# Kernel tuning notes

Hardware: AMD Instinct MI355X
Metric: run time of the kernel (lower is better)

## Reference

```python
import jax, jax.numpy as jnp
import numpy as np

D, DC, DR, NH = 2048, 512, 64, 16
HD = D // NH
B, T = 2, 2048


def _rope_tables(sl, off, dr):
    inv = 1.0 / (10000.0 ** (jnp.arange(0, dr, 2, dtype=jnp.float32) / dr))
    t = jnp.arange(off, off + sl, dtype=jnp.float32)
    f = jnp.outer(t, inv)                      # [sl, dr/2]
    e = jnp.concatenate([f, f], -1)            # [sl, dr]
    return jnp.cos(e), jnp.sin(e)


def _rap(x, c, s):
    d = x.shape[-1]
    x1, x2 = x[..., : d // 2], x[..., d // 2:]
    ch, sh = c[..., : d // 2], s[..., : d // 2]
    return jnp.concatenate([x1 * ch - x2 * sh, x2 * ch + x1 * sh], -1)


def setup_inputs() -> dict:
    key = jax.random.key(0)
    ks = jax.random.split(key, 8)
    def w(k, i, o):
        return jax.random.normal(k, (i, o), jnp.float32) * (1.0 / np.sqrt(i))
    return {
        "x": jax.random.normal(ks[0], (B, T, D), jnp.float32),
        "Wkv": w(ks[1], D, DC),    # kv_down
        "Wkup": w(ks[2], DC, D),   # k_up
        "Wvup": w(ks[3], DC, D),   # v_up
        "Wq": w(ks[4], D, D),      # q_proj
        "Wqr": w(ks[5], D, DR),    # q_rope
        "Wkr": w(ks[6], DC, DR),   # k_rope
        "Wo": w(ks[7], D, D),      # o_proj
    }


def reference(x, Wkv, Wkup, Wvup, Wq, Wqr, Wkr, Wo):
    Bx, Tx, d = x.shape
    offset = 0
    ckv = x @ Wkv                                   # [B,T,dc]
    kr = ckv @ Wkr                                  # [B,T,dr]
    cos, sin = _rope_tables(Tx, offset, DR)         # [T,dr]
    kr = _rap(kr, cos[None], sin[None])
    entry = jnp.concatenate([ckv, kr], -1)          # [B,T,dc+dr] (kv cache entry)
    tl = entry.shape[1]

    k = (ckv @ Wkup).reshape(Bx, tl, NH, HD).transpose(0, 2, 1, 3)   # [B,H,tl,hd]
    v = (ckv @ Wvup).reshape(Bx, tl, NH, HD).transpose(0, 2, 1, 3)
    q = (x @ Wq).reshape(Bx, Tx, NH, HD).transpose(0, 2, 1, 3)        # [B,H,T,hd]

    qr = _rap(x @ Wqr, cos[None], sin[None])        # [B,T,dr]

    ac = jnp.einsum("bhtd,bhsd->bhts", q, k)        # content scores
    ar = jnp.einsum("btd,bsd->bts", qr, kr)         # shared RoPE scores (same per head)
    scale = np.sqrt(HD + DR).astype(np.float32)
    scores = (ac + ar[:, None]) / scale             # [B,H,T,tl]

    # causal mask: triu(-inf, diagonal=tl-T+1)
    i = jnp.arange(Tx)[:, None]
    j = jnp.arange(tl)[None, :]
    mask = j > i + (tl - Tx)
    scores = jnp.where(mask[None, None], -jnp.inf, scores)

    attn = jax.nn.softmax(scores, -1)
    out = jnp.einsum("bhts,bhsd->bhtd", attn, v).transpose(0, 2, 1, 3).reshape(Bx, Tx, -1)
    return out @ Wo, entry
```

## Files before the change

### kernel.cpp

```cpp
#include <hip/hip_runtime.h>
#include <math.h>
#include <type_traits>

#define D    2048
#define DC   512
#define DR   64
#define NH   16
#define HD   128
#define Bb   2
#define Tt   2048
#define ROWS (Bb*Tt)
#define LDX  2176

typedef __bf16 bf16x8 __attribute__((ext_vector_type(8)));
typedef __bf16 bf16x4 __attribute__((ext_vector_type(4)));
typedef float  f32x4  __attribute__((ext_vector_type(4)));

typedef const void __attribute__((address_space(1))) gvoid;
typedef void       __attribute__((address_space(3))) lvoid;

__device__ __forceinline__ void load_lds16(const void* g, void* l) {
    __builtin_amdgcn_global_load_lds((gvoid*)g, (lvoid*)l, 16, 0, 0);
}

template <bool WF32, bool WBF16>
__global__ __launch_bounds__(256)
void gemm_bt(const __bf16* __restrict__ A, const __bf16* __restrict__ BT,
             float* __restrict__ Cf, __bf16* __restrict__ Cb,
             int M, int K, int ldcf, int ldcb) {
    __shared__ __bf16 As[128 * 32];
    __shared__ __bf16 Bs[128 * 32];

    const int tid  = threadIdx.x;
    const int w    = tid >> 6;
    const int lane = tid & 63;
    const int quad = lane >> 4;
    const int lc   = lane & 15;
    const int bm   = blockIdx.y * 128;
    const int bn   = blockIdx.x * 128;
    const int wm   = (w & 1) * 64;
    const int wn   = (w >> 1) * 64;

    const int sr = w * 32 + (lane >> 2);
    const int sc = (lane & 3) * 8;

    f32x4 acc[4][4] = {};

    for (int k0 = 0; k0 < K; k0 += 32) {
        const __bf16* ga = A  + (size_t)(bm + sr) * K + k0 + sc;
        const __bf16* gb = BT + (size_t)(bn + sr) * K + k0 + sc;
        load_lds16(ga,                  &As[(w * 32) * 32]);
        load_lds16(ga + (size_t)16 * K, &As[(w * 32 + 16) * 32]);
        load_lds16(gb,                  &Bs[(w * 32) * 32]);
        load_lds16(gb + (size_t)16 * K, &Bs[(w * 32 + 16) * 32]);
        __syncthreads();

        bf16x8 af[4], bfr[4];
        #pragma unroll
        for (int mi = 0; mi < 4; ++mi)
            af[mi] = *(bf16x8*)&As[(wm + mi * 16 + lc) * 32 + quad * 8];
        #pragma unroll
        for (int ni = 0; ni < 4; ++ni)
            bfr[ni] = *(bf16x8*)&Bs[(wn + ni * 16 + lc) * 32 + quad * 8];
        #pragma unroll
        for (int mi = 0; mi < 4; ++mi)
            #pragma unroll
            for (int ni = 0; ni < 4; ++ni)
                acc[mi][ni] = __builtin_amdgcn_mfma_f32_16x16x32_bf16(
                    af[mi], bfr[ni], acc[mi][ni], 0, 0, 0);
        __syncthreads();
    }

    #pragma unroll
    for (int mi = 0; mi < 4; ++mi)
        #pragma unroll
        for (int r = 0; r < 4; ++r) {
            const int row = bm + wm + mi * 16 + quad * 4 + r;
            const int col = bn + wn + lc;
            #pragma unroll
            for (int ni = 0; ni < 4; ++ni) {
                float v = acc[mi][ni][r];
                if constexpr (WF32)  Cf[(size_t)row * ldcf + col + ni * 16] = v;
                if constexpr (WBF16) Cb[(size_t)row * ldcb + col + ni * 16] = (__bf16)v;
            }
        }
}

__global__ void f32_to_bf16(const float* __restrict__ in,
                            __bf16* __restrict__ out, int n) {
    int i = blockIdx.x * blockDim.x + threadIdx.x;
    if (i < n) out[i] = (__bf16)in[i];
}

__global__ __launch_bounds__(256)
void transpose_conv(const float* __restrict__ W, __bf16* __restrict__ WT,
                    int R, int C) {
    __shared__ float tile[64][65];
    const int r0 = blockIdx.x * 64;
    const int c0 = blockIdx.y * 64;
    const int tid = threadIdx.x;
    for (int e = tid; e < 64 * 64; e += 256) {
        int i = e >> 6, j = e & 63;
        tile[i][j] = W[(size_t)(r0 + i) * C + c0 + j];
    }
    __syncthreads();
    for (int e = tid; e < 64 * 64; e += 256) {
        int i = e >> 6, j = e & 63;
        WT[(size_t)(c0 + i) * R + r0 + j] = (__bf16)tile[j][i];
    }
}

__global__ void rope_ext(__bf16* __restrict__ p, float* __restrict__ ent) {
    int idx = blockIdx.x * blockDim.x + threadIdx.x;
    if (idx >= ROWS * 32) return;
    int row = idx >> 5;
    int i   = idx & 31;
    int t   = row & (Tt - 1);
    float inv  = powf(10000.0f, -(float)(2 * i) / 64.0f);
    float fr   = (float)t * inv;
    float c = cosf(fr), s = sinf(fr);
    __bf16* v = p + (size_t)row * LDX + 2048;
    float x1 = (float)v[i], x2 = (float)v[i + 32];
    float o1 = x1 * c - x2 * s;
    float o2 = x2 * c + x1 * s;
    v[i]      = (__bf16)o1;
    v[i + 32] = (__bf16)o2;
    if (ent) {
        ent[(size_t)row * 576 + 512 + i] = o1;
        ent[(size_t)row * 576 + 544 + i] = o2;
    }
}

__global__ __launch_bounds__(256)
void transpose_v(const __bf16* __restrict__ vb, __bf16* __restrict__ vtb) {
    __shared__ __bf16 tile[64][65];
    const int t0 = blockIdx.x * 64;
    const int c0 = blockIdx.y * 64;
    const int b  = blockIdx.z;
    const int tid = threadIdx.x;
    for (int e = tid; e < 64 * 64; e += 256) {
        int i = e >> 6, j = e & 63;
        tile[i][j] = vb[((size_t)(b * Tt + t0 + i)) * D + c0 + j];
    }
    __syncthreads();
    for (int e = tid; e < 64 * 64; e += 256) {
        int i = e >> 6, j = e & 63;
        vtb[((size_t)(b * D + c0 + i)) * Tt + t0 + j] = tile[j][i];
    }
}

#define KS_STR 200
#define VT_STR 72
#define PS_STR 72
#define SPLIT_TILES 8

__device__ __forceinline__ int pbase_qt(int qt) {
    int a = qt >> 3, r = qt & 7;
    return qt + 4 * a * (a - 1) + a * r;
}

__global__ __launch_bounds__(256, 3)
void attn_split(const __bf16* __restrict__ qx, const __bf16* __restrict__ kx,
                const __bf16* __restrict__ vtb, __bf16* __restrict__ opart,
                float* __restrict__ mlpart) {
    const int qt = (Tt / 64 - 1) - (int)blockIdx.y;
    const int sp = blockIdx.x;
    const int t0 = sp * SPLIT_TILES;
    if (t0 > qt) return;
    const int tend = min(t0 + SPLIT_TILES, qt + 1);
    const int hb = blockIdx.z;
    const int h  = hb & (NH - 1);
    const int b  = hb >> 4;
    const int q0 = qt * 64;

    __shared__ __bf16 Ks[64][KS_STR];
    __shared__ __bf16 Vt[128][VT_STR];
    __shared__ __bf16 PsT[4][16][PS_STR];

    const int tid  = threadIdx.x;
    const int w    = tid >> 6;
    const int lane = tid & 63;
    const int quad = lane >> 4;
    const int lc   = lane & 15;

    bf16x8 aq[6];
    {
        const __bf16* qrow = qx + (size_t)(b * Tt + q0 + w * 16 + lc) * LDX;
        #pragma unroll
        for (int kt = 0; kt < 4; ++kt)
            aq[kt] = *(const bf16x8*)(qrow + h * HD + kt * 32 + quad * 8);
        #pragma unroll
        for (int kt = 0; kt < 2; ++kt)
            aq[4 + kt] = *(const bf16x8*)(qrow + 2048 + kt * 32 + quad * 8);
    }

    int krow[6], kcol[6], kgo[6];
    #pragma unroll
    for (int j = 0; j < 6; ++j) {
        int c   = tid + j * 256;
        int row = c / 24, c24 = c - row * 24;
        krow[j] = row;
        kcol[j] = c24 * 8;
        kgo[j]  = row * LDX + ((c24 < 16) ? (h * HD + c24 * 8)
                                          : (2048 + (c24 - 16) * 8));
    }
    const int vrow = tid >> 3;
    const int vcol = (tid & 7) * 8;
    const __bf16* kb0 = kx + (size_t)b * Tt * LDX;
    const __bf16* vb0 = vtb + ((size_t)b * D + (size_t)h * HD) * Tt;

    bf16x8 pk[6], pvv[4];
    {
        const __bf16* kbt = kb0 + (size_t)(t0 * 64) * LDX;
        const __bf16* vbt = vb0 + t0 * 64;
        #pragma unroll
        for (int j = 0; j < 6; ++j) pk[j] = *(const bf16x8*)(kbt + kgo[j]);
        #pragma unroll
        for (int j = 0; j < 4; ++j)
            pvv[j] = *(const bf16x8*)(vbt + (vrow + j * 32) * Tt + vcol);
    }

    float m_i = -1e30f, l_i = 0.f;
    f32x4 Of[8];
    #pragma unroll
    for (int n = 0; n < 8; ++n) Of[n] = (f32x4){0.f, 0.f, 0.f, 0.f};

    const float rscale = 0.07216878364870323f;
    const int qglob = q0 + w * 16 + lc;

    for (int it = t0; it < tend; ++it) {
        const int s0 = it * 64;
        __syncthreads();
        #pragma unroll
        for (int j = 0; j < 6; ++j) *(bf16x8*)&Ks[krow[j]][kcol[j]] = pk[j];
        #pragma unroll
        for (int j = 0; j < 4; ++j) *(bf16x8*)&Vt[vrow + j * 32][vcol] = pvv[j];
        __syncthreads();

        if (it + 1 < tend) {
            const __bf16* kbn = kb0 + (size_t)(s0 + 64) * LDX;
            const __bf16* vbn = vb0 + (s0 + 64);
            #pragma unroll
            for (int j = 0; j < 6; ++j) pk[j] = *(const bf16x8*)(kbn + kgo[j]);
            #pragma unroll
            for (int j = 0; j < 4; ++j)
                pvv[j] = *(const bf16x8*)(vbn + (vrow + j * 32) * Tt + vcol);
        }

        f32x4 st[4];
        #pragma unroll
        for (int f = 0; f < 4; ++f) st[f] = (f32x4){0.f, 0.f, 0.f, 0.f};
        #pragma unroll
        for (int kt = 0; kt < 6; ++kt) {
            #pragma unroll
            for (int f = 0; f < 4; ++f) {
                bf16x8 ak = *(bf16x8*)&Ks[f * 16 + lc][kt * 32 + quad * 8];
                st[f] = __builtin_amdgcn_mfma_f32_16x16x32_bf16(ak, aq[kt], st[f], 0, 0, 0);
            }
        }

        const bool dm = (it == qt);
        float mt = -1e30f;
        #pragma unroll
        for (int f = 0; f < 4; ++f)
            #pragma unroll
            for (int r = 0; r < 4; ++r) {
                float sv = st[f][r] * rscale;
                if (dm && (s0 + f * 16 + quad * 4 + r > qglob)) sv = -1e30f;
                st[f][r] = sv;
                mt = fmaxf(mt, sv);
            }
        mt = fmaxf(mt, __shfl_xor(mt, 16, 64));
        mt = fmaxf(mt, __shfl_xor(mt, 32, 64));
        float mn = fmaxf(m_i, mt);
        float al = __expf(m_i - mn);
        m_i = mn;
        float rsum = 0.f;
        #pragma unroll
        for (int f = 0; f < 4; ++f) {
            bf16x4 pr;
            #pragma unroll
            for (int r = 0; r < 4; ++r) {
                __bf16 pb = (__bf16)__expf(st[f][r] - mn);
                pr[r] = pb;
                rsum += (float)pb;
            }
            *(bf16x4*)&PsT[w][lc][f * 16 + quad * 4] = pr;
        }
        rsum += __shfl_xor(rsum, 16, 64);
        rsum += __shfl_xor(rsum, 32, 64);
        l_i = l_i * al + rsum;
        #pragma unroll
        for (int n = 0; n < 8; ++n)
            #pragma unroll
            for (int r = 0; r < 4; ++r) Of[n][r] *= al;

        #pragma unroll
        for (int kt = 0; kt < 2; ++kt) {
            bf16x8 bp = *(bf16x8*)&PsT[w][lc][kt * 32 + quad * 8];
            #pragma unroll
            for (int n = 0; n < 8; ++n) {
                bf16x8 av = *(bf16x8*)&Vt[n * 16 + lc][kt * 32 + quad * 8];
                Of[n] = __builtin_amdgcn_mfma_f32_16x16x32_bf16(av, bp, Of[n], 0, 0, 0);
            }
        }
    }

    const int p = hb * 80 + pbase_qt(qt) + sp;
    __bf16* ob = opart + (size_t)p * (64 * 128) + (size_t)(w * 16 + lc) * 128;
    #pragma unroll
    for (int n = 0; n < 8; ++n) {
        bf16x4 o4;
        #pragma unroll
        for (int r = 0; r < 4; ++r) o4[r] = (__bf16)Of[n][r];
        *(bf16x4*)(ob + n * 16 + quad * 4) = o4;
    }
    if (quad == 0) {
        mlpart[(size_t)p * 128 + w * 16 + lc]      = m_i;
        mlpart[(size_t)p * 128 + 64 + w * 16 + lc] = l_i;
    }
}

__global__ __launch_bounds__(256)
void attn_reduce(const __bf16* __restrict__ opart, const float* __restrict__ mlpart,
                 __bf16* __restrict__ aob) {
    const int qt = blockIdx.x;
    const int hb = blockIdx.y;
    const int h  = hb & (NH - 1);
    const int b  = hb >> 4;
    const int nsp = (qt >> 3) + 1;
    const int p0  = hb * 80 + pbase_qt(qt);
    const int tid = threadIdx.x;
    const int ql  = tid >> 2;
    const int cg  = (tid & 3) * 32;

    float M = -1e30f;
    for (int s = 0; s < nsp; ++s)
        M = fmaxf(M, mlpart[(size_t)(p0 + s) * 128 + ql]);
    float L = 0.f;
    float acc[32];
    #pragma unroll
    for (int j = 0; j < 32; ++j) acc[j] = 0.f;
    for (int s = 0; s < nsp; ++s) {
        float ms = mlpart[(size_t)(p0 + s) * 128 + ql];
        float ls = mlpart[(size_t)(p0 + s) * 128 + 64 + ql];
        float sc = __expf(ms - M);
        L += ls * sc;
        const __bf16* op = opart + (size_t)(p0 + s) * (64 * 128) + (size_t)ql * 128 + cg;
        #pragma unroll
        for (int j8 = 0; j8 < 4; ++j8) {
            bf16x8 v = *(const bf16x8*)(op + j8 * 8);
            #pragma unroll
            for (int e = 0; e < 8; ++e) acc[j8 * 8 + e] += sc * (float)v[e];
        }
    }
    float invL = 1.0f / L;
    __bf16* outp = aob + ((size_t)(b * Tt + qt * 64 + ql)) * D + h * HD + cg;
    #pragma unroll
    for (int j8 = 0; j8 < 4; ++j8) {
        bf16x8 v;
        #pragma unroll
        for (int e = 0; e < 8; ++e) v[e] = (__bf16)(acc[j8 * 8 + e] * invL);
        *(bf16x8*)(outp + j8 * 8) = v;
    }
}

extern "C" void kernel_launch(void* const* d_in, const int* in_sizes, int n_in,
                              void* d_out, int out_size, void* d_ws, size_t ws_size,
                              hipStream_t stream) {
    const float* x    = (const float*)d_in[0];
    const float* Wkv  = (const float*)d_in[1];
    const float* Wkup = (const float*)d_in[2];
    const float* Wvup = (const float*)d_in[3];
    const float* Wq   = (const float*)d_in[4];
    const float* Wqr  = (const float*)d_in[5];
    const float* Wkr  = (const float*)d_in[6];
    const float* Wo   = (const float*)d_in[7];

    float* out0 = (float*)d_out;
    float* out1 = out0 + (size_t)ROWS * D;

    char* wsb = (char*)d_ws;
    __bf16* qext = (__bf16*)wsb;  wsb += (size_t)ROWS * LDX * 2;
    __bf16* kext = (__bf16*)wsb;  wsb += (size_t)ROWS * LDX * 2;
    __bf16* vtb  = (__bf16*)wsb;  wsb += (size_t)ROWS * D   * 2;
    __bf16* aob  = (__bf16*)wsb;  wsb += (size_t)ROWS * D   * 2;
    __bf16* WoT  = (__bf16*)wsb;  wsb += (size_t)D * D * 2;

    char* scratch = wsb;
    __bf16* xb    = (__bf16*)scratch;
    __bf16* vb    = (__bf16*)(scratch + 16777216);
    __bf16* ckvb  = (__bf16*)(scratch + 33554432);
    __bf16* WkvT  = (__bf16*)(scratch + 37748736);
    __bf16* WqxT  = (__bf16*)(scratch + 39845888);
    __bf16* KupxT = (__bf16*)(scratch + 48758784);
    __bf16* WvupT = (__bf16*)(scratch + 50987008);
    __bf16* opart  = (__bf16*)scratch;
    float*  mlpart = (float*)(scratch + (size_t)2560 * 64 * 128 * 2);

    dim3 blk(256);

    f32_to_bf16<<<(ROWS * D + 255) / 256, blk, 0, stream>>>(x, xb, ROWS * D);
    transpose_conv<<<dim3(D / 64, DC / 64), blk, 0, stream>>>(Wkv, WkvT, D, DC);
    transpose_conv<<<dim3(D / 64, D / 64),  blk, 0, stream>>>(Wq, WqxT, D, D);
    transpose_conv<<<dim3(D / 64, 1),       blk, 0, stream>>>(Wqr, WqxT + (size_t)D * D, D, DR);
    transpose_conv<<<dim3(DC / 64, D / 64), blk, 0, stream>>>(Wkup, KupxT, DC, D);
    transpose_conv<<<dim3(DC / 64, 1),      blk, 0, stream>>>(Wkr, KupxT + (size_t)D * DC, DC, DR);
    transpose_conv<<<dim3(DC / 64, D / 64), blk, 0, stream>>>(Wvup, WvupT, DC, D);
    transpose_conv<<<dim3(D / 64, D / 64),  blk, 0, stream>>>(Wo, WoT, D, D);

    gemm_bt<true, true><<<dim3(DC / 128, ROWS / 128), blk, 0, stream>>>(
        xb, WkvT, out1, ckvb, ROWS, D, 576, DC);

    gemm_bt<false, true><<<dim3(LDX / 128, ROWS / 128), blk, 0, stream>>>(
        xb, WqxT, (float*)nullptr, qext, ROWS, D, 0, LDX);
    rope_ext<<<(ROWS * 32 + 255) / 256, blk, 0, stream>>>(qext, (float*)nullptr);

    gemm_bt<false, true><<<dim3(LDX / 128, ROWS / 128), blk, 0, stream>>>(
        ckvb, KupxT, (float*)nullptr, kext, ROWS, DC, 0, LDX);
    rope_ext<<<(ROWS * 32 + 255) / 256, blk, 0, stream>>>(kext, out1);

    gemm_bt<false, true><<<dim3(D / 128, ROWS / 128), blk, 0, stream>>>(
        ckvb, WvupT, (float*)nullptr, vb, ROWS, DC, 0, D);
    transpose_v<<<dim3(Tt / 64, D / 64, Bb), blk, 0, stream>>>(vb, vtb);

    attn_split<<<dim3(4, Tt / 64, NH * Bb), blk, 0, stream>>>(
        qext, kext, vtb, opart, mlpart);
    attn_reduce<<<dim3(Tt / 64, NH * Bb), blk, 0, stream>>>(opart, mlpart, aob);

    gemm_bt<true, false><<<dim3(D / 128, ROWS / 128), blk, 0, stream>>>(
        aob, WoT, out0, (__bf16*)nullptr, ROWS, D, D, 0);
}
```

Baseline: 553.9 us.

## Use 128-row query tiles with 32x32x16 MFMA in split attention

The split-KV attention kernel now processes 128 query rows per block (32 per wave) instead of 64, so each K/V tile loaded into LDS is reused across twice as many queries. It switches from 16x16x32 to 32x32x16 MFMA instructions, adds s_setprio around the MFMA sections, and skips fully masked tiles per wave. The partial buffers and the reduce kernel are resized for 128-row tiles. In exchange there is higher register pressure (launch bounds drop from 3 to 2 blocks per CU) and fewer blocks in the grid.

```diff
diff --git a/kernel.cpp b/kernel.cpp
--- a/kernel.cpp
+++ b/kernel.cpp
@@ -15,6 +15,8 @@
 typedef __bf16 bf16x8 __attribute__((ext_vector_type(8)));
 typedef __bf16 bf16x4 __attribute__((ext_vector_type(4)));
 typedef float  f32x4  __attribute__((ext_vector_type(4)));
+typedef float  f32x16 __attribute__((ext_vector_type(16)));
+typedef unsigned int uint;
 
 typedef const void __attribute__((address_space(1))) gvoid;
 typedef void       __attribute__((address_space(3))) lvoid;
@@ -155,43 +157,50 @@
 #define SPLIT_TILES 8
 
 __device__ __forceinline__ int pbase_qt(int qt) {
-    int a = qt >> 3, r = qt & 7;
-    return qt + 4 * a * (a - 1) + a * r;
-}
-
-__global__ __launch_bounds__(256, 3)
+    int a = qt >> 2, r = qt & 3;
+    return qt + 2 * a * (a - 1) + r * a;
+}
+
+__global__ __launch_bounds__(256, 2)
 void attn_split(const __bf16* __restrict__ qx, const __bf16* __restrict__ kx,
                 const __bf16* __restrict__ vtb, __bf16* __restrict__ opart,
                 float* __restrict__ mlpart) {
-    const int qt = (Tt / 64 - 1) - (int)blockIdx.y;
+    const int qt = (Tt / 128 - 1) - (int)blockIdx.y;
     const int sp = blockIdx.x;
     const int t0 = sp * SPLIT_TILES;
-    if (t0 > qt) return;
-    const int tend = min(t0 + SPLIT_TILES, qt + 1);
+    const int ntiles = 2 * qt + 2;
+    if (t0 >= ntiles) return;
+    const int tend = min(t0 + SPLIT_TILES, ntiles);
     const int hb = blockIdx.z;
     const int h  = hb & (NH - 1);
     const int b  = hb >> 4;
-    const int q0 = qt * 64;
+    const int q0 = qt * 128;
 
     __shared__ __bf16 Ks[64][KS_STR];
     __shared__ __bf16 Vt[128][VT_STR];
-    __shared__ __bf16 PsT[4][16][PS_STR];
-
-    const int tid  = threadIdx.x;
-    const int w    = tid >> 6;
-    const int lane = tid & 63;
-    const int quad = lane >> 4;
-    const int lc   = lane & 15;
-
-    bf16x8 aq[6];
+    __shared__ __bf16 PsT[4][32][PS_STR];
+
+    const int tid    = threadIdx.x;
+    const int w      = tid >> 6;
+    const int lane   = tid & 63;
+    const int lane31 = lane & 31;
+    const int hi     = lane >> 5;
+    const int hi8    = hi * 8;
+    const int hi4    = hi * 4;
+
+    const int qwmax = q0 + w * 32 + 31;
+    const int tendw = min(tend, (qwmax >> 6) + 1);
+    const int qglob = q0 + w * 32 + lane31;
+
+    bf16x8 aq[12];
     {
-        const __bf16* qrow = qx + (size_t)(b * Tt + q0 + w * 16 + lc) * LDX;
+        const __bf16* qrow = qx + (size_t)(b * Tt + q0 + w * 32 + lane31) * LDX;
+        #pragma unroll
+        for (int kt = 0; kt < 8; ++kt)
+            aq[kt] = *(const bf16x8*)(qrow + h * HD + kt * 16 + hi8);
         #pragma unroll
         for (int kt = 0; kt < 4; ++kt)
-            aq[kt] = *(const bf16x8*)(qrow + h * HD + kt * 32 + quad * 8);
-        #pragma unroll
-        for (int kt = 0; kt < 2; ++kt)
-            aq[4 + kt] = *(const bf16x8*)(qrow + 2048 + kt * 32 + quad * 8);
+            aq[8 + kt] = *(const bf16x8*)(qrow + 2048 + kt * 16 + hi8);
     }
 
     int krow[6], kcol[6], kgo[6];
@@ -221,12 +230,9 @@
     }
 
     float m_i = -1e30f, l_i = 0.f;
-    f32x4 Of[8];
-    #pragma unroll
-    for (int n = 0; n < 8; ++n) Of[n] = (f32x4){0.f, 0.f, 0.f, 0.f};
+    f32x16 Of[4] = {};
 
     const float rscale = 0.07216878364870323f;
-    const int qglob = q0 + w * 16 + lc;
 
     for (int it = t0; it < tend; ++it) {
         const int s0 = it * 64;
@@ -247,77 +253,95 @@
                 pvv[j] = *(const bf16x8*)(vbn + (vrow + j * 32) * Tt + vcol);
         }
 
-        f32x4 st[4];
-        #pragma unroll
-        for (int f = 0; f < 4; ++f) st[f] = (f32x4){0.f, 0.f, 0.f, 0.f};
-        #pragma unroll
-        for (int kt = 0; kt < 6; ++kt) {
-            #pragma unroll
-            for (int f = 0; f < 4; ++f) {
-                bf16x8 ak = *(bf16x8*)&Ks[f * 16 + lc][kt * 32 + quad * 8];
-                st[f] = __builtin_amdgcn_mfma_f32_16x16x32_bf16(ak, aq[kt], st[f], 0, 0, 0);
-            }
+        if (it < tendw) {
+            f32x16 st0 = {}, st1 = {};
+            __builtin_amdgcn_s_setprio(1);
+            #pragma unroll
+            for (int kt = 0; kt < 12; ++kt) {
+                bf16x8 ak0 = *(bf16x8*)&Ks[lane31][kt * 16 + hi8];
+                bf16x8 ak1 = *(bf16x8*)&Ks[32 + lane31][kt * 16 + hi8];
+                st0 = __builtin_amdgcn_mfma_f32_32x32x16_bf16(ak0, aq[kt], st0, 0, 0, 0);
+                st1 = __builtin_amdgcn_mfma_f32_32x32x16_bf16(ak1, aq[kt], st1, 0, 0, 0);
+            }
+            __builtin_amdgcn_s_setprio(0);
+
+            const bool dm = (s0 + 63 > q0 + w * 32);
+            float sv0[16], sv1[16];
+            float mt = -1e30f;
+            #pragma unroll
+            for (int r = 0; r < 16; ++r) {
+                float a0 = st0[r] * rscale;
+                float a1 = st1[r] * rscale;
+                if (dm) {
+                    int kr = (r & 3) + 8 * (r >> 2) + hi4;
+                    if (s0 + kr > qglob)      a0 = -1e30f;
+                    if (s0 + 32 + kr > qglob) a1 = -1e30f;
+                }
+                sv0[r] = a0; sv1[r] = a1;
+                mt = fmaxf(mt, fmaxf(a0, a1));
+            }
+            mt = fmaxf(mt, __shfl_xor(mt, 32, 64));
+
+            float mn = fmaxf(m_i, mt);
+            float al = __expf(m_i - mn);
+            m_i = mn;
+
+            float rsum = 0.f;
+            #pragma unroll
+            for (int g = 0; g < 4; ++g) {
+                bf16x4 pr;
+                #pragma unroll
+                for (int j = 0; j < 4; ++j) {
+                    __bf16 pb = (__bf16)__expf(sv0[g * 4 + j] - mn);
+                    pr[j] = pb;
+                    rsum += (float)pb;
+                }
+                *(bf16x4*)&PsT[w][lane31][g * 8 + hi4] = pr;
+            }
+            #pragma unroll
+            for (int g = 0; g < 4; ++g) {
+                bf16x4 pr;
+                #pragma unroll
+                for (int j = 0; j < 4; ++j) {
+                    __bf16 pb = (__bf16)__expf(sv1[g * 4 + j] - mn);
+                    pr[j] = pb;
+                    rsum += (float)pb;
+                }
+                *(bf16x4*)&PsT[w][lane31][32 + g * 8 + hi4] = pr;
+            }
+            rsum += __shfl_xor(rsum, 32, 64);
+            l_i = l_i * al + rsum;
+            #pragma unroll
+            for (int nb = 0; nb < 4; ++nb) Of[nb] *= al;
+
+            __builtin_amdgcn_s_setprio(1);
+            #pragma unroll
+            for (int kblk = 0; kblk < 4; ++kblk) {
+                bf16x8 bp = *(bf16x8*)&PsT[w][lane31][kblk * 16 + hi8];
+                #pragma unroll
+                for (int nb = 0; nb < 4; ++nb) {
+                    bf16x8 av = *(bf16x8*)&Vt[nb * 32 + lane31][kblk * 16 + hi8];
+                    Of[nb] = __builtin_amdgcn_mfma_f32_32x32x16_bf16(av, bp, Of[nb], 0, 0, 0);
+                }
+            }
+            __builtin_amdgcn_s_setprio(0);
         }
-
-        const bool dm = (it == qt);
-        float mt = -1e30f;
-        #pragma unroll
-        for (int f = 0; f < 4; ++f)
-            #pragma unroll
-            for (int r = 0; r < 4; ++r) {
-                float sv = st[f][r] * rscale;
-                if (dm && (s0 + f * 16 + quad * 4 + r > qglob)) sv = -1e30f;
-                st[f][r] = sv;
-                mt = fmaxf(mt, sv);
-            }
-        mt = fmaxf(mt, __shfl_xor(mt, 16, 64));
-        mt = fmaxf(mt, __shfl_xor(mt, 32, 64));
-        float mn = fmaxf(m_i, mt);
-        float al = __expf(m_i - mn);
-        m_i = mn;
-        float rsum = 0.f;
-        #pragma unroll
-        for (int f = 0; f < 4; ++f) {
-            bf16x4 pr;
-            #pragma unroll
-            for (int r = 0; r < 4; ++r) {
-                __bf16 pb = (__bf16)__expf(st[f][r] - mn);
-                pr[r] = pb;
-                rsum += (float)pb;
-            }
-            *(bf16x4*)&PsT[w][lc][f * 16 + quad * 4] = pr;
+    }
+
+    const int p = hb * 40 + pbase_qt(qt) + sp;
+    __bf16* ob = opart + (size_t)p * (128 * 128) + (size_t)(w * 32 + lane31) * 128;
+    #pragma unroll
+    for (int nb = 0; nb < 4; ++nb)
+        #pragma unroll
+        for (int g = 0; g < 4; ++g) {
+            bf16x4 o4;
+            #pragma unroll
+            for (int j = 0; j < 4; ++j) o4[j] = (__bf16)Of[nb][g * 4 + j];
+            *(bf16x4*)(ob + nb * 32 + g * 8 + hi4) = o4;
         }
-        rsum += __shfl_xor(rsum, 16, 64);
-        rsum += __shfl_xor(rsum, 32, 64);
-        l_i = l_i * al + rsum;
-        #pragma unroll
-        for (int n = 0; n < 8; ++n)
-            #pragma unroll
-            for (int r = 0; r < 4; ++r) Of[n][r] *= al;
-
-        #pragma unroll
-        for (int kt = 0; kt < 2; ++kt) {
-            bf16x8 bp = *(bf16x8*)&PsT[w][lc][kt * 32 + quad * 8];
-            #pragma unroll
-            for (int n = 0; n < 8; ++n) {
-                bf16x8 av = *(bf16x8*)&Vt[n * 16 + lc][kt * 32 + quad * 8];
-                Of[n] = __builtin_amdgcn_mfma_f32_16x16x32_bf16(av, bp, Of[n], 0, 0, 0);
-            }
-        }
-    }
-
-    const int p = hb * 80 + pbase_qt(qt) + sp;
-    __bf16* ob = opart + (size_t)p * (64 * 128) + (size_t)(w * 16 + lc) * 128;
-    #pragma unroll
-    for (int n = 0; n < 8; ++n) {
-        bf16x4 o4;
-        #pragma unroll
-        for (int r = 0; r < 4; ++r) o4[r] = (__bf16)Of[n][r];
-        *(bf16x4*)(ob + n * 16 + quad * 4) = o4;
-    }
-    if (quad == 0) {
-        mlpart[(size_t)p * 128 + w * 16 + lc]      = m_i;
-        mlpart[(size_t)p * 128 + 64 + w * 16 + lc] = l_i;
+    if (hi == 0) {
+        mlpart[(size_t)p * 256 + w * 32 + lane31]       = m_i;
+        mlpart[(size_t)p * 256 + 128 + w * 32 + lane31] = l_i;
     }
 }
 
@@ -328,36 +352,36 @@
     const int hb = blockIdx.y;
     const int h  = hb & (NH - 1);
     const int b  = hb >> 4;
-    const int nsp = (qt >> 3) + 1;
-    const int p0  = hb * 80 + pbase_qt(qt);
+    const int nsp = (qt >> 2) + 1;
+    const int p0  = hb * 40 + pbase_qt(qt);
     const int tid = threadIdx.x;
-    const int ql  = tid >> 2;
-    const int cg  = (tid & 3) * 32;
+    const int ql  = tid >> 1;
+    const int cg  = (tid & 1) * 64;
 
     float M = -1e30f;
     for (int s = 0; s < nsp; ++s)
-        M = fmaxf(M, mlpart[(size_t)(p0 + s) * 128 + ql]);
+        M = fmaxf(M, mlpart[(size_t)(p0 + s) * 256 + ql]);
     float L = 0.f;
-    float acc[32];
+    float acc[64];
     #pragma unroll
-    for (int j = 0; j < 32; ++j) acc[j] = 0.f;
+    for (int j = 0; j < 64; ++j) acc[j] = 0.f;
     for (int s = 0; s < nsp; ++s) {
-        float ms = mlpart[(size_t)(p0 + s) * 128 + ql];
-        float ls = mlpart[(size_t)(p0 + s) * 128 + 64 + ql];
+        float ms = mlpart[(size_t)(p0 + s) * 256 + ql];
+        float ls = mlpart[(size_t)(p0 + s) * 256 + 128 + ql];
         float sc = __expf(ms - M);
         L += ls * sc;
-        const __bf16* op = opart + (size_t)(p0 + s) * (64 * 128) + (size_t)ql * 128 + cg;
-        #pragma unroll
-        for (int j8 = 0; j8 < 4; ++j8) {
+        const __bf16* op = opart + (size_t)(p0 + s) * (128 * 128) + (size_t)ql * 128 + cg;
+        #pragma unroll
+        for (int j8 = 0; j8 < 8; ++j8) {
             bf16x8 v = *(const bf16x8*)(op + j8 * 8);
             #pragma unroll
             for (int e = 0; e < 8; ++e) acc[j8 * 8 + e] += sc * (float)v[e];
         }
     }
     float invL = 1.0f / L;
-    __bf16* outp = aob + ((size_t)(b * Tt + qt * 64 + ql)) * D + h * HD + cg;
+    __bf16* outp = aob + ((size_t)(b * Tt + qt * 128 + ql)) * D + h * HD + cg;
     #pragma unroll
-    for (int j8 = 0; j8 < 4; ++j8) {
+    for (int j8 = 0; j8 < 8; ++j8) {
         bf16x8 v;
         #pragma unroll
         for (int e = 0; e < 8; ++e) v[e] = (__bf16)(acc[j8 * 8 + e] * invL);
@@ -396,7 +420,7 @@
     __bf16* KupxT = (__bf16*)(scratch + 48758784);
     __bf16* WvupT = (__bf16*)(scratch + 50987008);
     __bf16* opart  = (__bf16*)scratch;
-    float*  mlpart = (float*)(scratch + (size_t)2560 * 64 * 128 * 2);
+    float*  mlpart = (float*)(scratch + (size_t)1280 * 128 * 128 * 2);
 
     dim3 blk(256);
 
@@ -424,9 +448,9 @@
         ckvb, WvupT, (float*)nullptr, vb, ROWS, DC, 0, D);
     transpose_v<<<dim3(Tt / 64, D / 64, Bb), blk, 0, stream>>>(vb, vtb);
 
-    attn_split<<<dim3(4, Tt / 64, NH * Bb), blk, 0, stream>>>(
+    attn_split<<<dim3(4, Tt / 128, NH * Bb), blk, 0, stream>>>(
         qext, kext, vtb, opart, mlpart);
-    attn_reduce<<<dim3(Tt / 64, NH * Bb), blk, 0, stream>>>(opart, mlpart, aob);
+    attn_reduce<<<dim3(Tt / 128, NH * Bb), blk, 0, stream>>>(opart, mlpart, aob);
 
     gemm_bt<true, false><<<dim3(D / 128, ROWS / 128), blk, 0, stream>>>(
         aob, WoT, out0, (__bf16*)nullptr, ROWS, D, D, 0);
```

After: 527.5 us. 4.8% less time.
